# Optimization experiments

Hardware: AMD Instinct MI355X
Metric: run time of the kernel (lower is better)

## Reference

```python
import jax, jax.numpy as jnp
import numpy as np

MARGIN_SCALE = 0.2
SPATIAL_ALPHA = 0.6
CHANNEL_ALPHA = 0.5
LANG_ALPHA = 0.4
EPS = 1e-06


def _xywh_to_xyxy(boxes):
    xc, yc, w, h = jnp.split(boxes, 4, axis=-1)
    return jnp.concatenate([xc - w / 2.0, yc - h / 2.0, xc + w / 2.0, yc + h / 2.0], axis=-1)


def _clamp_boxes(boxes):
    x1, y1, x2, y2 = [jnp.clip(b[..., 0], 0.0, 1.0) for b in jnp.split(boxes, 4, axis=-1)]
    x_low, x_high = jnp.minimum(x1, x2), jnp.maximum(x1, x2)
    y_low, y_high = jnp.minimum(y1, y2), jnp.maximum(y1, y2)
    w = jnp.maximum(x_high - x_low, EPS)
    h = jnp.maximum(y_high - y_low, EPS)
    cx = (x_high + x_low) * 0.5
    cy = (y_high + y_low) * 0.5
    return jnp.stack([
        jnp.clip(cx - w * 0.5, 0.0, 1.0),
        jnp.clip(cy - h * 0.5, 0.0, 1.0),
        jnp.clip(cx + w * 0.5, 0.0, 1.0),
        jnp.clip(cy + h * 0.5, 0.0, 1.0),
    ], axis=-1)


def _box_to_mask(boxes_xyxy, H, W, margin, dtype):
    # fully vectorized replacement of the per-sample Python loop
    ys = jnp.linspace(0.0, 1.0, H)  # [H]
    xs = jnp.linspace(0.0, 1.0, W)  # [W]
    x1, y1, x2, y2 = [boxes_xyxy[:, i] for i in range(4)]
    mx1 = jnp.clip(x1 - margin, 0.0, 1.0)[:, None, None]
    my1 = jnp.clip(y1 - margin, 0.0, 1.0)[:, None, None]
    mx2 = jnp.clip(x2 + margin, 0.0, 1.0)[:, None, None]
    my2 = jnp.clip(y2 + margin, 0.0, 1.0)[:, None, None]
    xg = xs[None, None, :]  # [1,1,W]
    yg = ys[None, :, None]  # [1,H,1]
    mask = (xg >= mx1) & (xg <= mx2) & (yg >= my1) & (yg <= my2)  # [B,H,W]
    return mask.astype(dtype)[:, None, :, :]  # [B,1,H,W]


def _conv2d(x, w, b, pad):
    out = jax.lax.conv_general_dilated(
        x, w, window_strides=(1, 1), padding=((pad, pad), (pad, pad)),
        dimension_numbers=('NCHW', 'OIHW', 'NCHW'))
    return out + b[None, :, None, None]


def setup_inputs() -> dict:
    key = jax.random.key(0)
    ks = jax.random.split(key, 9)
    B, C, H, W = 32, 256, 64, 64
    s = lambda fan_in: 1.0 / np.sqrt(fan_in)
    return {
        'feat': jax.random.normal(ks[0], (B, C, H, W), jnp.float32),
        'lang_vec': jax.random.normal(ks[1], (B, 256), jnp.float32),
        'pointer_xywh': jax.random.uniform(ks[2], (B, 4), jnp.float32),
        'conv1_w': jax.random.normal(ks[3], (16, 1, 3, 3), jnp.float32) * s(9),
        'conv1_b': jnp.zeros((16,), jnp.float32),
        'conv2_w': jax.random.normal(ks[4], (1, 16, 1, 1), jnp.float32) * s(16),
        'conv2_b': jnp.zeros((1,), jnp.float32),
        'cg_w1': jax.random.normal(ks[5], (256, 512), jnp.float32) * s(512),
        'cg_b1': jnp.zeros((256,), jnp.float32),
        'cg_w2': jax.random.normal(ks[6], (256, 256), jnp.float32) * s(256),
        'cg_b2': jnp.zeros((256,), jnp.float32),
        'lf_w1': jax.random.normal(ks[7], (256, 512), jnp.float32) * s(512),
        'lf_b1': jnp.zeros((256,), jnp.float32),
        'lf_w2': jax.random.normal(ks[8], (256, 256), jnp.float32) * s(256),
        'lf_b2': jnp.zeros((256,), jnp.float32),
    }


def reference(feat, lang_vec, pointer_xywh, conv1_w, conv1_b, conv2_w, conv2_b,
              cg_w1, cg_b1, cg_w2, cg_b2, lf_w1, lf_b1, lf_w2, lf_b2):
    B, C, H, W = feat.shape
    boxes_xyxy = _clamp_boxes(_xywh_to_xyxy(pointer_xywh))
    w = jnp.maximum(boxes_xyxy[:, 2] - boxes_xyxy[:, 0], 1e-4)
    h = jnp.maximum(boxes_xyxy[:, 3] - boxes_xyxy[:, 1], 1e-4)
    diag = jnp.sqrt(w * w + h * h)
    margin = jnp.clip(diag * MARGIN_SCALE, 0.02, 0.2)
    mask = _box_to_mask(boxes_xyxy, H, W, margin, feat.dtype)  # [B,1,H,W]

    # spatial gate: conv3x3 -> relu -> conv1x1 -> sigmoid
    hidden = jax.nn.relu(_conv2d(mask, conv1_w, conv1_b, pad=1))
    refined_mask = jax.nn.sigmoid(_conv2d(hidden, conv2_w, conv2_b, pad=0))  # [B,1,H,W]

    mask_area = jnp.maximum(refined_mask.sum(axis=(2, 3)), 1.0)  # [B,1]
    pointer_feat = (feat * refined_mask).sum(axis=(2, 3)) / mask_area  # [B,C]

    fusion = jnp.concatenate([pointer_feat, lang_vec], axis=1)  # [B, C+256]
    ch_gate = jax.nn.sigmoid(jax.nn.relu(fusion @ cg_w1.T + cg_b1) @ cg_w2.T + cg_b2)
    ch_gate = ch_gate.reshape(B, C, 1, 1)
    lang_delta = jnp.tanh(jax.nn.relu(fusion @ lf_w1.T + lf_b1) @ lf_w2.T + lf_b2)

    guided_feat = feat * (1.0 + SPATIAL_ALPHA * refined_mask) * (1.0 + CHANNEL_ALPHA * ch_gate)
    guided_lang = lang_vec + LANG_ALPHA * lang_delta
    return (guided_feat, guided_lang, boxes_xyxy, refined_mask, pointer_feat)
```

## Files before the change

### kernel.cpp

```cpp
#include <hip/hip_runtime.h>
#include <math.h>

#define B_  32
#define C_  256
#define H_  64
#define W_  64
#define HW  (H_*W_)
#define HW4 (HW/4)
#define RPB 4

typedef float f32x4 __attribute__((ext_vector_type(4)));

__device__ __forceinline__ float clamp01(float v) {
    return fminf(fmaxf(v, 0.0f), 1.0f);
}

struct BoxParams {
    float bx1, by1, bx2, by2, mx1, my1, mx2, my2;
};

__device__ __forceinline__ BoxParams box_math(const float* __restrict__ xywh, int b) {
    const float xc = xywh[b * 4 + 0];
    const float yc = xywh[b * 4 + 1];
    const float bw = xywh[b * 4 + 2];
    const float bh = xywh[b * 4 + 3];

    float x1 = clamp01(xc - bw * 0.5f);
    float y1 = clamp01(yc - bh * 0.5f);
    float x2 = clamp01(xc + bw * 0.5f);
    float y2 = clamp01(yc + bh * 0.5f);
    float xl = fminf(x1, x2), xh = fmaxf(x1, x2);
    float yl = fminf(y1, y2), yh = fmaxf(y1, y2);
    float w_ = fmaxf(xh - xl, 1e-6f);
    float h_ = fmaxf(yh - yl, 1e-6f);
    float cx = (xh + xl) * 0.5f, cy = (yh + yl) * 0.5f;
    BoxParams p;
    p.bx1 = clamp01(cx - w_ * 0.5f);
    p.by1 = clamp01(cy - h_ * 0.5f);
    p.bx2 = clamp01(cx + w_ * 0.5f);
    p.by2 = clamp01(cy + h_ * 0.5f);
    float ww = fmaxf(p.bx2 - p.bx1, 1e-4f);
    float hh = fmaxf(p.by2 - p.by1, 1e-4f);
    float diag = sqrtf(ww * ww + hh * hh);
    float margin = fminf(fmaxf(diag * 0.2f, 0.02f), 0.2f);
    p.mx1 = clamp01(p.bx1 - margin);
    p.my1 = clamp01(p.by1 - margin);
    p.mx2 = clamp01(p.bx2 + margin);
    p.my2 = clamp01(p.by2 + margin);
    return p;
}

__device__ __forceinline__ void build_tables(
    int t, const BoxParams& p, float b2v,
    const float* sw1, const float* sb1, const float* sw2,
    int* xpat, int* ypat, float* tbl)
{
    if (t < 64) {
        const int x = t;
        int pp = 0;
        #pragma unroll
        for (int k = 0; k < 3; ++k) {
            const int xx = x + k - 1;
            float gx = (float)((double)xx / 63.0);
            bool in = (xx >= 0) && (xx < W_) && (gx >= p.mx1) && (gx <= p.mx2);
            pp |= (in ? 1 : 0) << k;
        }
        xpat[x] = pp;
    } else if (t < 128) {
        const int y = t - 64;
        int pp = 0;
        #pragma unroll
        for (int k = 0; k < 3; ++k) {
            const int yy = y + k - 1;
            float gy = (float)((double)yy / 63.0);
            bool in = (yy >= 0) && (yy < H_) && (gy >= p.my1) && (gy <= p.my2);
            pp |= (in ? 1 : 0) << k;
        }
        ypat[y] = pp;
    } else if (t < 192) {
        const int e = t - 128;
        const int xp = e & 7, yp = e >> 3;
        float mv[9];
        #pragma unroll
        for (int ky = 0; ky < 3; ++ky)
            #pragma unroll
            for (int kx = 0; kx < 3; ++kx)
                mv[ky * 3 + kx] = (((yp >> ky) & 1) && ((xp >> kx) & 1)) ? 1.0f : 0.0f;
        float z = b2v;
        #pragma unroll
        for (int oc = 0; oc < 16; ++oc) {
            float hsum = sb1[oc];
            #pragma unroll
            for (int k = 0; k < 9; ++k) hsum = fmaf(mv[k], sw1[oc * 9 + k], hsum);
            z = fmaf(fmaxf(hsum, 0.0f), sw2[oc], z);
        }
        tbl[e] = 1.0f / (1.0f + expf(-z));
    }
}

__global__ __launch_bounds__(256) void kern_pf(
    const float* __restrict__ feat, const float* __restrict__ xywh,
    const float* __restrict__ conv1_w, const float* __restrict__ conv1_b,
    const float* __restrict__ conv2_w, const float* __restrict__ conv2_b,
    float* __restrict__ out_boxes, float* __restrict__ out_rm,
    float* __restrict__ out_pf)
{
    const int blk = blockIdx.x;
    const int b = blk >> 6;
    const int g = blk & 63;
    const int c0 = g * RPB;
    const int t = threadIdx.x;

    __shared__ float sw1[16 * 9];
    __shared__ float sb1[16];
    __shared__ float sw2[16];
    __shared__ float tbl[64];
    __shared__ int   xpat[64];
    __shared__ int   ypat[64];
    __shared__ f32x4 rm4_lds[HW4];
    __shared__ float sreda[4];
    __shared__ f32x4 sredv[4];

    float* rm_lds = (float*)rm4_lds;

    if (t < 144)                 sw1[t]       = conv1_w[t];
    else if (t < 160)            sb1[t - 144] = conv1_b[t - 144];
    else if (t < 176)            sw2[t - 160] = conv2_w[t - 160];
    const float b2v = conv2_b[0];

    const BoxParams bp = box_math(xywh, b);
    if (t == 0 && g == 0) {
        out_boxes[b * 4 + 0] = bp.bx1;
        out_boxes[b * 4 + 1] = bp.by1;
        out_boxes[b * 4 + 2] = bp.bx2;
        out_boxes[b * 4 + 3] = bp.by2;
    }
    __syncthreads();

    build_tables(t, bp, b2v, sw1, sb1, sw2, xpat, ypat, tbl);
    __syncthreads();

    float asum = 0.0f;
    for (int p = t; p < HW; p += 256) {
        const int y = p >> 6;
        const int x = p & 63;
        float rm = tbl[ypat[y] * 8 + xpat[x]];
        rm_lds[p] = rm;
        asum += rm;
    }
    #pragma unroll
    for (int off = 32; off > 0; off >>= 1) asum += __shfl_down(asum, off, 64);
    const int lane = t & 63, wid = t >> 6;
    if (lane == 0) sreda[wid] = asum;
    __syncthreads();
    const float inv = 1.0f / fmaxf(sreda[0] + sreda[1] + sreda[2] + sreda[3], 1.0f);

    if (g == 0) {
        f32x4* orm = (f32x4*)(out_rm + (size_t)b * HW);
        for (int i = t; i < HW4; i += 256) orm[i] = rm4_lds[i];
    }

    const f32x4* fr = (const f32x4*)(feat + ((size_t)b * C_ + c0) * HW);
    float s0 = 0.f, s1 = 0.f, s2 = 0.f, s3 = 0.f;
    #pragma unroll 2
    for (int i = t; i < HW4; i += 256) {
        f32x4 r = rm4_lds[i];
        f32x4 f0 = fr[i];
        f32x4 f1 = fr[i + HW4];
        f32x4 f2 = fr[i + 2 * HW4];
        f32x4 f3 = fr[i + 3 * HW4];
        s0 = fmaf(f0.x, r.x, fmaf(f0.y, r.y, fmaf(f0.z, r.z, fmaf(f0.w, r.w, s0))));
        s1 = fmaf(f1.x, r.x, fmaf(f1.y, r.y, fmaf(f1.z, r.z, fmaf(f1.w, r.w, s1))));
        s2 = fmaf(f2.x, r.x, fmaf(f2.y, r.y, fmaf(f2.z, r.z, fmaf(f2.w, r.w, s2))));
        s3 = fmaf(f3.x, r.x, fmaf(f3.y, r.y, fmaf(f3.z, r.z, fmaf(f3.w, r.w, s3))));
    }
    #pragma unroll
    for (int off = 32; off > 0; off >>= 1) {
        s0 += __shfl_down(s0, off, 64);
        s1 += __shfl_down(s1, off, 64);
        s2 += __shfl_down(s2, off, 64);
        s3 += __shfl_down(s3, off, 64);
    }
    if (lane == 0) { f32x4 v; v.x = s0; v.y = s1; v.z = s2; v.w = s3; sredv[wid] = v; }
    __syncthreads();
    if (t == 0) {
        f32x4 t0 = sredv[0], t1 = sredv[1], t2 = sredv[2], t3 = sredv[3];
        out_pf[b * C_ + c0 + 0] = (t0.x + t1.x + t2.x + t3.x) * inv;
        out_pf[b * C_ + c0 + 1] = (t0.y + t1.y + t2.y + t3.y) * inv;
        out_pf[b * C_ + c0 + 2] = (t0.z + t1.z + t2.z + t3.z) * inv;
        out_pf[b * C_ + c0 + 3] = (t0.w + t1.w + t2.w + t3.w) * inv;
    }
}

__global__ __launch_bounds__(256) void kern_mlp(
    const float* __restrict__ pf, const float* __restrict__ lang,
    const float* __restrict__ cg_w1, const float* __restrict__ cg_b1,
    const float* __restrict__ cg_w2, const float* __restrict__ cg_b2,
    const float* __restrict__ lf_w1, const float* __restrict__ lf_b1,
    const float* __restrict__ lf_w2, const float* __restrict__ lf_b2,
    float* __restrict__ ws_cg, float* __restrict__ out_gl)
{
    const int b = blockIdx.x >> 1;
    const int which = blockIdx.x & 1;
    const int t = threadIdx.x;
    __shared__ float fus[512];
    __shared__ float hid[256];

    fus[t]       = pf[b * 256 + t];
    fus[256 + t] = lang[b * 256 + t];

    const float* w1 = which ? lf_w1 : cg_w1;
    const float* b1 = which ? lf_b1 : cg_b1;
    const float* w2 = which ? lf_w2 : cg_w2;
    const float* b2 = which ? lf_b2 : cg_b2;
    __syncthreads();

    const f32x4* wv = (const f32x4*)(w1 + (size_t)t * 512);
    const f32x4* fv = (const f32x4*)fus;
    float s = 0.0f;
    #pragma unroll 4
    for (int k = 0; k < 128; ++k) {
        f32x4 f = fv[k], w = wv[k];
        s = fmaf(f.x, w.x, fmaf(f.y, w.y, fmaf(f.z, w.z, fmaf(f.w, w.w, s))));
    }
    hid[t] = fmaxf(s + b1[t], 0.0f);
    __syncthreads();

    const f32x4* w2v = (const f32x4*)(w2 + (size_t)t * 256);
    const f32x4* hv = (const f32x4*)hid;
    float s2 = 0.0f;
    #pragma unroll 4
    for (int k = 0; k < 64; ++k) {
        f32x4 h = hv[k], w = w2v[k];
        s2 = fmaf(h.x, w.x, fmaf(h.y, w.y, fmaf(h.z, w.z, fmaf(h.w, w.w, s2))));
    }
    s2 += b2[t];
    if (which == 0) {
        ws_cg[b * 256 + t] = 1.0f + 0.5f / (1.0f + expf(-s2));
    } else {
        out_gl[b * 256 + t] = fus[256 + t] + 0.4f * tanhf(s2);
    }
}

__global__ __launch_bounds__(256) void kern_guided(
    const float* __restrict__ feat, const float* __restrict__ rm,
    const float* __restrict__ ws_cg, float* __restrict__ out_gf)
{
    const int blk = blockIdx.x;
    const int b = blk >> 6;
    const int c0 = (blk & 63) * RPB;
    const float g0 = ws_cg[b * C_ + c0 + 0];
    const float g1 = ws_cg[b * C_ + c0 + 1];
    const float g2 = ws_cg[b * C_ + c0 + 2];
    const float g3 = ws_cg[b * C_ + c0 + 3];

    const size_t row0 = ((size_t)b * C_ + c0) * HW;
    const f32x4* fr = (const f32x4*)(feat + row0);
    f32x4* orow = (f32x4*)(out_gf + row0);
    const f32x4* r4 = (const f32x4*)(rm + (size_t)b * HW);

    #pragma unroll 2
    for (int i = threadIdx.x; i < HW4; i += 256) {
        f32x4 r = r4[i];
        f32x4 m;
        m.x = 1.0f + 0.6f * r.x;
        m.y = 1.0f + 0.6f * r.y;
        m.z = 1.0f + 0.6f * r.z;
        m.w = 1.0f + 0.6f * r.w;
        f32x4 f0 = fr[i];
        f32x4 f1 = fr[i + HW4];
        f32x4 f2 = fr[i + 2 * HW4];
        f32x4 f3 = fr[i + 3 * HW4];
        f32x4 o0, o1, o2, o3;
        o0.x = f0.x * m.x * g0; o0.y = f0.y * m.y * g0;
        o0.z = f0.z * m.z * g0; o0.w = f0.w * m.w * g0;
        o1.x = f1.x * m.x * g1; o1.y = f1.y * m.y * g1;
        o1.z = f1.z * m.z * g1; o1.w = f1.w * m.w * g1;
        o2.x = f2.x * m.x * g2; o2.y = f2.y * m.y * g2;
        o2.z = f2.z * m.z * g2; o2.w = f2.w * m.w * g2;
        o3.x = f3.x * m.x * g3; o3.y = f3.y * m.y * g3;
        o3.z = f3.z * m.z * g3; o3.w = f3.w * m.w * g3;
        orow[i]           = o0;
        orow[i + HW4]     = o1;
        orow[i + 2*HW4]   = o2;
        orow[i + 3*HW4]   = o3;
    }
}

extern "C" void kernel_launch(void* const* d_in, const int* in_sizes, int n_in,
                              void* d_out, int out_size, void* d_ws, size_t ws_size,
                              hipStream_t stream) {
    const float* feat     = (const float*)d_in[0];
    const float* lang     = (const float*)d_in[1];
    const float* xywh     = (const float*)d_in[2];
    const float* conv1_w  = (const float*)d_in[3];
    const float* conv1_b  = (const float*)d_in[4];
    const float* conv2_w  = (const float*)d_in[5];
    const float* conv2_b  = (const float*)d_in[6];
    const float* cg_w1    = (const float*)d_in[7];
    const float* cg_b1    = (const float*)d_in[8];
    const float* cg_w2    = (const float*)d_in[9];
    const float* cg_b2    = (const float*)d_in[10];
    const float* lf_w1    = (const float*)d_in[11];
    const float* lf_b1    = (const float*)d_in[12];
    const float* lf_w2    = (const float*)d_in[13];
    const float* lf_b2    = (const float*)d_in[14];

    float* out = (float*)d_out;
    const size_t N_GF = (size_t)B_ * C_ * HW;
    float* out_gf    = out;
    float* out_gl    = out_gf + N_GF;
    float* out_boxes = out_gl + (size_t)B_ * C_;
    float* out_rm    = out_boxes + B_ * 4;
    float* out_pf    = out_rm + (size_t)B_ * HW;

    float* wsf   = (float*)d_ws;
    float* ws_cg = wsf;

    (void)ws_size; (void)in_sizes; (void)n_in; (void)out_size;

    kern_pf<<<B_ * C_ / RPB, 256, 0, stream>>>(feat, xywh,
                                               conv1_w, conv1_b, conv2_w, conv2_b,
                                               out_boxes, out_rm, out_pf);
    kern_mlp<<<B_ * 2, 256, 0, stream>>>(out_pf, lang,
                                         cg_w1, cg_b1, cg_w2, cg_b2,
                                         lf_w1, lf_b1, lf_w2, lf_b2,
                                         ws_cg, out_gl);
    kern_guided<<<B_ * C_ / RPB, 256, 0, stream>>>(feat, out_rm, ws_cg, out_gf);
}
```

Measured before the change: 96.61 us.

## Split mask into separate kernel, swizzle block order, use nontemporal stores

Moves refined-mask construction and area reduction into a small kernel that writes the mask and per-quarter partial sums to global memory, so the pointer-feature kernel reads the mask from memory instead of rebuilding it in LDS in every block. Both feat-streaming kernels remap block indices so that consecutive blocks land on different batches, and the loops are fully unrolled with more loads in flight. The guided-output kernel writes with nontemporal stores so the large output does not pollute cache. The cost is one extra kernel launch and a global round trip for the mask, and the swizzle may hurt cache reuse of the shared mask row.

```diff
diff --git a/kernel.cpp b/kernel.cpp
--- a/kernel.cpp
+++ b/kernel.cpp
@@ -13,6 +13,10 @@
 
 __device__ __forceinline__ float clamp01(float v) {
     return fminf(fmaxf(v, 0.0f), 1.0f);
+}
+
+__device__ __forceinline__ int swz2048(int blk) {
+    return (blk & 7) * 256 + (blk >> 3);
 }
 
 struct BoxParams {
@@ -98,17 +102,15 @@
     }
 }
 
-__global__ __launch_bounds__(256) void kern_pf(
-    const float* __restrict__ feat, const float* __restrict__ xywh,
+__global__ __launch_bounds__(256) void kern_mask(
+    const float* __restrict__ xywh,
     const float* __restrict__ conv1_w, const float* __restrict__ conv1_b,
     const float* __restrict__ conv2_w, const float* __restrict__ conv2_b,
     float* __restrict__ out_boxes, float* __restrict__ out_rm,
-    float* __restrict__ out_pf)
-{
-    const int blk = blockIdx.x;
-    const int b = blk >> 6;
-    const int g = blk & 63;
-    const int c0 = g * RPB;
+    float* __restrict__ ws_part)
+{
+    const int b = blockIdx.x >> 2;
+    const int q = blockIdx.x & 3;
     const int t = threadIdx.x;
 
     __shared__ float sw1[16 * 9];
@@ -117,11 +119,7 @@
     __shared__ float tbl[64];
     __shared__ int   xpat[64];
     __shared__ int   ypat[64];
-    __shared__ f32x4 rm4_lds[HW4];
-    __shared__ float sreda[4];
-    __shared__ f32x4 sredv[4];
-
-    float* rm_lds = (float*)rm4_lds;
+    __shared__ float sred[4];
 
     if (t < 144)                 sw1[t]       = conv1_w[t];
     else if (t < 160)            sb1[t - 144] = conv1_b[t - 144];
@@ -129,7 +127,7 @@
     const float b2v = conv2_b[0];
 
     const BoxParams bp = box_math(xywh, b);
-    if (t == 0 && g == 0) {
+    if (t == 0 && q == 0) {
         out_boxes[b * 4 + 0] = bp.bx1;
         out_boxes[b * 4 + 1] = bp.by1;
         out_boxes[b * 4 + 2] = bp.bx2;
@@ -141,39 +139,61 @@
     __syncthreads();
 
     float asum = 0.0f;
-    for (int p = t; p < HW; p += 256) {
+    const int p0 = q * 1024;
+    for (int pi = t; pi < 1024; pi += 256) {
+        const int p = p0 + pi;
         const int y = p >> 6;
         const int x = p & 63;
         float rm = tbl[ypat[y] * 8 + xpat[x]];
-        rm_lds[p] = rm;
+        out_rm[b * HW + p] = rm;
         asum += rm;
     }
     #pragma unroll
     for (int off = 32; off > 0; off >>= 1) asum += __shfl_down(asum, off, 64);
-    const int lane = t & 63, wid = t >> 6;
-    if (lane == 0) sreda[wid] = asum;
-    __syncthreads();
-    const float inv = 1.0f / fmaxf(sreda[0] + sreda[1] + sreda[2] + sreda[3], 1.0f);
-
-    if (g == 0) {
-        f32x4* orm = (f32x4*)(out_rm + (size_t)b * HW);
-        for (int i = t; i < HW4; i += 256) orm[i] = rm4_lds[i];
-    }
+    int lane = t & 63, wid = t >> 6;
+    if (lane == 0) sred[wid] = asum;
+    __syncthreads();
+    if (t == 0) ws_part[b * 4 + q] = sred[0] + sred[1] + sred[2] + sred[3];
+}
+
+__global__ __launch_bounds__(256) void kern_pf(
+    const float* __restrict__ feat, const float* __restrict__ rm,
+    const float* __restrict__ ws_part, float* __restrict__ out_pf)
+{
+    const int job = swz2048(blockIdx.x);
+    const int b = job >> 6;
+    const int c0 = (job & 63) * RPB;
+    const int t = threadIdx.x;
+    __shared__ f32x4 sredv[4];
 
     const f32x4* fr = (const f32x4*)(feat + ((size_t)b * C_ + c0) * HW);
+    const f32x4* r4 = (const f32x4*)(rm + (size_t)b * HW);
+
     float s0 = 0.f, s1 = 0.f, s2 = 0.f, s3 = 0.f;
-    #pragma unroll 2
-    for (int i = t; i < HW4; i += 256) {
-        f32x4 r = rm4_lds[i];
-        f32x4 f0 = fr[i];
-        f32x4 f1 = fr[i + HW4];
-        f32x4 f2 = fr[i + 2 * HW4];
-        f32x4 f3 = fr[i + 3 * HW4];
-        s0 = fmaf(f0.x, r.x, fmaf(f0.y, r.y, fmaf(f0.z, r.z, fmaf(f0.w, r.w, s0))));
-        s1 = fmaf(f1.x, r.x, fmaf(f1.y, r.y, fmaf(f1.z, r.z, fmaf(f1.w, r.w, s1))));
-        s2 = fmaf(f2.x, r.x, fmaf(f2.y, r.y, fmaf(f2.z, r.z, fmaf(f2.w, r.w, s2))));
-        s3 = fmaf(f3.x, r.x, fmaf(f3.y, r.y, fmaf(f3.z, r.z, fmaf(f3.w, r.w, s3))));
-    }
+    #pragma unroll
+    for (int k = 0; k < 2; ++k) {
+        const int i0 = t + k * 512;
+        const int i1 = i0 + 256;
+        f32x4 ra = r4[i0];
+        f32x4 rb = r4[i1];
+        f32x4 a0 = fr[i0];
+        f32x4 a1 = fr[i0 + HW4];
+        f32x4 a2 = fr[i0 + 2 * HW4];
+        f32x4 a3 = fr[i0 + 3 * HW4];
+        f32x4 b0 = fr[i1];
+        f32x4 b1 = fr[i1 + HW4];
+        f32x4 b2 = fr[i1 + 2 * HW4];
+        f32x4 b3 = fr[i1 + 3 * HW4];
+        s0 = fmaf(a0.x, ra.x, fmaf(a0.y, ra.y, fmaf(a0.z, ra.z, fmaf(a0.w, ra.w, s0))));
+        s1 = fmaf(a1.x, ra.x, fmaf(a1.y, ra.y, fmaf(a1.z, ra.z, fmaf(a1.w, ra.w, s1))));
+        s2 = fmaf(a2.x, ra.x, fmaf(a2.y, ra.y, fmaf(a2.z, ra.z, fmaf(a2.w, ra.w, s2))));
+        s3 = fmaf(a3.x, ra.x, fmaf(a3.y, ra.y, fmaf(a3.z, ra.z, fmaf(a3.w, ra.w, s3))));
+        s0 = fmaf(b0.x, rb.x, fmaf(b0.y, rb.y, fmaf(b0.z, rb.z, fmaf(b0.w, rb.w, s0))));
+        s1 = fmaf(b1.x, rb.x, fmaf(b1.y, rb.y, fmaf(b1.z, rb.z, fmaf(b1.w, rb.w, s1))));
+        s2 = fmaf(b2.x, rb.x, fmaf(b2.y, rb.y, fmaf(b2.z, rb.z, fmaf(b2.w, rb.w, s2))));
+        s3 = fmaf(b3.x, rb.x, fmaf(b3.y, rb.y, fmaf(b3.z, rb.z, fmaf(b3.w, rb.w, s3))));
+    }
+
     #pragma unroll
     for (int off = 32; off > 0; off >>= 1) {
         s0 += __shfl_down(s0, off, 64);
@@ -181,9 +201,13 @@
         s2 += __shfl_down(s2, off, 64);
         s3 += __shfl_down(s3, off, 64);
     }
+    const int lane = t & 63, wid = t >> 6;
     if (lane == 0) { f32x4 v; v.x = s0; v.y = s1; v.z = s2; v.w = s3; sredv[wid] = v; }
     __syncthreads();
     if (t == 0) {
+        float area = fmaxf(ws_part[b * 4 + 0] + ws_part[b * 4 + 1] +
+                           ws_part[b * 4 + 2] + ws_part[b * 4 + 3], 1.0f);
+        float inv = 1.0f / area;
         f32x4 t0 = sredv[0], t1 = sredv[1], t2 = sredv[2], t3 = sredv[3];
         out_pf[b * C_ + c0 + 0] = (t0.x + t1.x + t2.x + t3.x) * inv;
         out_pf[b * C_ + c0 + 1] = (t0.y + t1.y + t2.y + t3.y) * inv;
@@ -246,9 +270,10 @@
     const float* __restrict__ feat, const float* __restrict__ rm,
     const float* __restrict__ ws_cg, float* __restrict__ out_gf)
 {
-    const int blk = blockIdx.x;
-    const int b = blk >> 6;
-    const int c0 = (blk & 63) * RPB;
+    const int job = swz2048(blockIdx.x);
+    const int b = job >> 6;
+    const int c0 = (job & 63) * RPB;
+    const int t = threadIdx.x;
     const float g0 = ws_cg[b * C_ + c0 + 0];
     const float g1 = ws_cg[b * C_ + c0 + 1];
     const float g2 = ws_cg[b * C_ + c0 + 2];
@@ -259,31 +284,52 @@
     f32x4* orow = (f32x4*)(out_gf + row0);
     const f32x4* r4 = (const f32x4*)(rm + (size_t)b * HW);
 
-    #pragma unroll 2
-    for (int i = threadIdx.x; i < HW4; i += 256) {
-        f32x4 r = r4[i];
-        f32x4 m;
-        m.x = 1.0f + 0.6f * r.x;
-        m.y = 1.0f + 0.6f * r.y;
-        m.z = 1.0f + 0.6f * r.z;
-        m.w = 1.0f + 0.6f * r.w;
-        f32x4 f0 = fr[i];
-        f32x4 f1 = fr[i + HW4];
-        f32x4 f2 = fr[i + 2 * HW4];
-        f32x4 f3 = fr[i + 3 * HW4];
-        f32x4 o0, o1, o2, o3;
-        o0.x = f0.x * m.x * g0; o0.y = f0.y * m.y * g0;
-        o0.z = f0.z * m.z * g0; o0.w = f0.w * m.w * g0;
-        o1.x = f1.x * m.x * g1; o1.y = f1.y * m.y * g1;
-        o1.z = f1.z * m.z * g1; o1.w = f1.w * m.w * g1;
-        o2.x = f2.x * m.x * g2; o2.y = f2.y * m.y * g2;
-        o2.z = f2.z * m.z * g2; o2.w = f2.w * m.w * g2;
-        o3.x = f3.x * m.x * g3; o3.y = f3.y * m.y * g3;
-        o3.z = f3.z * m.z * g3; o3.w = f3.w * m.w * g3;
-        orow[i]           = o0;
-        orow[i + HW4]     = o1;
-        orow[i + 2*HW4]   = o2;
-        orow[i + 3*HW4]   = o3;
+    #pragma unroll
+    for (int k = 0; k < 2; ++k) {
+        const int i0 = t + k * 512;
+        const int i1 = i0 + 256;
+        f32x4 ra = r4[i0];
+        f32x4 rb = r4[i1];
+        f32x4 a0 = fr[i0];
+        f32x4 a1 = fr[i0 + HW4];
+        f32x4 a2 = fr[i0 + 2 * HW4];
+        f32x4 a3 = fr[i0 + 3 * HW4];
+        f32x4 b0 = fr[i1];
+        f32x4 b1 = fr[i1 + HW4];
+        f32x4 b2 = fr[i1 + 2 * HW4];
+        f32x4 b3 = fr[i1 + 3 * HW4];
+
+        f32x4 ma, mb;
+        ma.x = 1.0f + 0.6f * ra.x; ma.y = 1.0f + 0.6f * ra.y;
+        ma.z = 1.0f + 0.6f * ra.z; ma.w = 1.0f + 0.6f * ra.w;
+        mb.x = 1.0f + 0.6f * rb.x; mb.y = 1.0f + 0.6f * rb.y;
+        mb.z = 1.0f + 0.6f * rb.z; mb.w = 1.0f + 0.6f * rb.w;
+
+        f32x4 o;
+        o.x = a0.x * ma.x * g0; o.y = a0.y * ma.y * g0;
+        o.z = a0.z * ma.z * g0; o.w = a0.w * ma.w * g0;
+        __builtin_nontemporal_store(o, &orow[i0]);
+        o.x = a1.x * ma.x * g1; o.y = a1.y * ma.y * g1;
+        o.z = a1.z * ma.z * g1; o.w = a1.w * ma.w * g1;
+        __builtin_nontemporal_store(o, &orow[i0 + HW4]);
+        o.x = a2.x * ma.x * g2; o.y = a2.y * ma.y * g2;
+        o.z = a2.z * ma.z * g2; o.w = a2.w * ma.w * g2;
+        __builtin_nontemporal_store(o, &orow[i0 + 2 * HW4]);
+        o.x = a3.x * ma.x * g3; o.y = a3.y * ma.y * g3;
+        o.z = a3.z * ma.z * g3; o.w = a3.w * ma.w * g3;
+        __builtin_nontemporal_store(o, &orow[i0 + 3 * HW4]);
+        o.x = b0.x * mb.x * g0; o.y = b0.y * mb.y * g0;
+        o.z = b0.z * mb.z * g0; o.w = b0.w * mb.w * g0;
+        __builtin_nontemporal_store(o, &orow[i1]);
+        o.x = b1.x * mb.x * g1; o.y = b1.y * mb.y * g1;
+        o.z = b1.z * mb.z * g1; o.w = b1.w * mb.w * g1;
+        __builtin_nontemporal_store(o, &orow[i1 + HW4]);
+        o.x = b2.x * mb.x * g2; o.y = b2.y * mb.y * g2;
+        o.z = b2.z * mb.z * g2; o.w = b2.w * mb.w * g2;
+        __builtin_nontemporal_store(o, &orow[i1 + 2 * HW4]);
+        o.x = b3.x * mb.x * g3; o.y = b3.y * mb.y * g3;
+        o.z = b3.z * mb.z * g3; o.w = b3.w * mb.w * g3;
+        __builtin_nontemporal_store(o, &orow[i1 + 3 * HW4]);
     }
 }
 
@@ -314,14 +360,15 @@
     float* out_rm    = out_boxes + B_ * 4;
     float* out_pf    = out_rm + (size_t)B_ * HW;
 
-    float* wsf   = (float*)d_ws;
-    float* ws_cg = wsf;
+    float* wsf     = (float*)d_ws;
+    float* ws_part = wsf;
+    float* ws_cg   = wsf + 128;
 
     (void)ws_size; (void)in_sizes; (void)n_in; (void)out_size;
 
-    kern_pf<<<B_ * C_ / RPB, 256, 0, stream>>>(feat, xywh,
-                                               conv1_w, conv1_b, conv2_w, conv2_b,
-                                               out_boxes, out_rm, out_pf);
+    kern_mask<<<B_ * 4, 256, 0, stream>>>(xywh, conv1_w, conv1_b, conv2_w, conv2_b,
+                                          out_boxes, out_rm, ws_part);
+    kern_pf<<<B_ * C_ / RPB, 256, 0, stream>>>(feat, out_rm, ws_part, out_pf);
     kern_mlp<<<B_ * 2, 256, 0, stream>>>(out_pf, lang,
                                          cg_w1, cg_b1, cg_w2, cg_b2,
                                          lf_w1, lf_b1, lf_w2, lf_b2,
```

Measured after the change: 102.0 us. +5.6%, slower.

## Recompute refined mask in guided kernel and use nontemporal stores

Applied to the files above, without the earlier changes.

The guided kernel now rebuilds the refined mask in LDS from the box parameters and conv weights instead of reading it back from global memory, precomputing 1+0.6*rm. Both the pointer-feature and guided loops are fully unrolled so each thread issues all 16 feature loads up front, and the output writes use nontemporal stores to limit cache pollution. This costs extra per-block setup (table build plus LDS fill and syncs) and more registers in exchange for more loads in flight and less global traffic.

```diff
diff --git a/kernel.cpp b/kernel.cpp
--- a/kernel.cpp
+++ b/kernel.cpp
@@ -98,6 +98,20 @@
     }
 }
 
+__device__ __forceinline__ float fill_rm(
+    int t, const int* xpat, const int* ypat, const float* tbl, float* rm_lds)
+{
+    float asum = 0.0f;
+    for (int p = t; p < HW; p += 256) {
+        const int y = p >> 6;
+        const int x = p & 63;
+        float rm = tbl[ypat[y] * 8 + xpat[x]];
+        rm_lds[p] = rm;
+        asum += rm;
+    }
+    return asum;
+}
+
 __global__ __launch_bounds__(256) void kern_pf(
     const float* __restrict__ feat, const float* __restrict__ xywh,
     const float* __restrict__ conv1_w, const float* __restrict__ conv1_b,
@@ -140,14 +154,7 @@
     build_tables(t, bp, b2v, sw1, sb1, sw2, xpat, ypat, tbl);
     __syncthreads();
 
-    float asum = 0.0f;
-    for (int p = t; p < HW; p += 256) {
-        const int y = p >> 6;
-        const int x = p & 63;
-        float rm = tbl[ypat[y] * 8 + xpat[x]];
-        rm_lds[p] = rm;
-        asum += rm;
-    }
+    float asum = fill_rm(t, xpat, ypat, tbl, rm_lds);
     #pragma unroll
     for (int off = 32; off > 0; off >>= 1) asum += __shfl_down(asum, off, 64);
     const int lane = t & 63, wid = t >> 6;
@@ -160,20 +167,27 @@
         for (int i = t; i < HW4; i += 256) orm[i] = rm4_lds[i];
     }
 
-    const f32x4* fr = (const f32x4*)(feat + ((size_t)b * C_ + c0) * HW);
+    const f32x4* fs = (const f32x4*)(feat + ((size_t)b * C_ + c0) * HW);
     float s0 = 0.f, s1 = 0.f, s2 = 0.f, s3 = 0.f;
-    #pragma unroll 2
-    for (int i = t; i < HW4; i += 256) {
-        f32x4 r = rm4_lds[i];
-        f32x4 f0 = fr[i];
-        f32x4 f1 = fr[i + HW4];
-        f32x4 f2 = fr[i + 2 * HW4];
-        f32x4 f3 = fr[i + 3 * HW4];
-        s0 = fmaf(f0.x, r.x, fmaf(f0.y, r.y, fmaf(f0.z, r.z, fmaf(f0.w, r.w, s0))));
-        s1 = fmaf(f1.x, r.x, fmaf(f1.y, r.y, fmaf(f1.z, r.z, fmaf(f1.w, r.w, s1))));
-        s2 = fmaf(f2.x, r.x, fmaf(f2.y, r.y, fmaf(f2.z, r.z, fmaf(f2.w, r.w, s2))));
-        s3 = fmaf(f3.x, r.x, fmaf(f3.y, r.y, fmaf(f3.z, r.z, fmaf(f3.w, r.w, s3))));
-    }
+    #pragma unroll
+    for (int r = 0; r < 4; ++r) {
+        f32x4 f0 = fs[t + (r * 4 + 0) * 256];
+        f32x4 f1 = fs[t + (r * 4 + 1) * 256];
+        f32x4 f2 = fs[t + (r * 4 + 2) * 256];
+        f32x4 f3 = fs[t + (r * 4 + 3) * 256];
+        f32x4 r0 = rm4_lds[t];
+        f32x4 r1 = rm4_lds[t + 256];
+        f32x4 r2 = rm4_lds[t + 512];
+        f32x4 r3 = rm4_lds[t + 768];
+        float acc = 0.0f;
+        acc = fmaf(f0.x, r0.x, fmaf(f0.y, r0.y, fmaf(f0.z, r0.z, fmaf(f0.w, r0.w, acc))));
+        acc = fmaf(f1.x, r1.x, fmaf(f1.y, r1.y, fmaf(f1.z, r1.z, fmaf(f1.w, r1.w, acc))));
+        acc = fmaf(f2.x, r2.x, fmaf(f2.y, r2.y, fmaf(f2.z, r2.z, fmaf(f2.w, r2.w, acc))));
+        acc = fmaf(f3.x, r3.x, fmaf(f3.y, r3.y, fmaf(f3.z, r3.z, fmaf(f3.w, r3.w, acc))));
+        if (r == 0) s0 = acc; else if (r == 1) s1 = acc;
+        else if (r == 2) s2 = acc; else s3 = acc;
+    }
+
     #pragma unroll
     for (int off = 32; off > 0; off >>= 1) {
         s0 += __shfl_down(s0, off, 64);
@@ -243,47 +257,75 @@
 }
 
 __global__ __launch_bounds__(256) void kern_guided(
-    const float* __restrict__ feat, const float* __restrict__ rm,
+    const float* __restrict__ feat, const float* __restrict__ xywh,
+    const float* __restrict__ conv1_w, const float* __restrict__ conv1_b,
+    const float* __restrict__ conv2_w, const float* __restrict__ conv2_b,
     const float* __restrict__ ws_cg, float* __restrict__ out_gf)
 {
     const int blk = blockIdx.x;
     const int b = blk >> 6;
     const int c0 = (blk & 63) * RPB;
+    const int t = threadIdx.x;
+
+    __shared__ float sw1[16 * 9];
+    __shared__ float sb1[16];
+    __shared__ float sw2[16];
+    __shared__ float tbl[64];
+    __shared__ int   xpat[64];
+    __shared__ int   ypat[64];
+    __shared__ f32x4 rm4_lds[HW4];
+
+    float* rm_lds = (float*)rm4_lds;
+
+    if (t < 144)                 sw1[t]       = conv1_w[t];
+    else if (t < 160)            sb1[t - 144] = conv1_b[t - 144];
+    else if (t < 176)            sw2[t - 160] = conv2_w[t - 160];
+    const float b2v = conv2_b[0];
+
+    const BoxParams bp = box_math(xywh, b);
+    __syncthreads();
+    build_tables(t, bp, b2v, sw1, sb1, sw2, xpat, ypat, tbl);
+    __syncthreads();
+    for (int p = t; p < HW; p += 256) {
+        const int y = p >> 6;
+        const int x = p & 63;
+        rm_lds[p] = 1.0f + 0.6f * tbl[ypat[y] * 8 + xpat[x]];
+    }
+    __syncthreads();
+
     const float g0 = ws_cg[b * C_ + c0 + 0];
     const float g1 = ws_cg[b * C_ + c0 + 1];
     const float g2 = ws_cg[b * C_ + c0 + 2];
     const float g3 = ws_cg[b * C_ + c0 + 3];
 
     const size_t row0 = ((size_t)b * C_ + c0) * HW;
-    const f32x4* fr = (const f32x4*)(feat + row0);
-    f32x4* orow = (f32x4*)(out_gf + row0);
-    const f32x4* r4 = (const f32x4*)(rm + (size_t)b * HW);
-
-    #pragma unroll 2
-    for (int i = threadIdx.x; i < HW4; i += 256) {
-        f32x4 r = r4[i];
-        f32x4 m;
-        m.x = 1.0f + 0.6f * r.x;
-        m.y = 1.0f + 0.6f * r.y;
-        m.z = 1.0f + 0.6f * r.z;
-        m.w = 1.0f + 0.6f * r.w;
-        f32x4 f0 = fr[i];
-        f32x4 f1 = fr[i + HW4];
-        f32x4 f2 = fr[i + 2 * HW4];
-        f32x4 f3 = fr[i + 3 * HW4];
-        f32x4 o0, o1, o2, o3;
-        o0.x = f0.x * m.x * g0; o0.y = f0.y * m.y * g0;
-        o0.z = f0.z * m.z * g0; o0.w = f0.w * m.w * g0;
-        o1.x = f1.x * m.x * g1; o1.y = f1.y * m.y * g1;
-        o1.z = f1.z * m.z * g1; o1.w = f1.w * m.w * g1;
-        o2.x = f2.x * m.x * g2; o2.y = f2.y * m.y * g2;
-        o2.z = f2.z * m.z * g2; o2.w = f2.w * m.w * g2;
-        o3.x = f3.x * m.x * g3; o3.y = f3.y * m.y * g3;
-        o3.z = f3.z * m.z * g3; o3.w = f3.w * m.w * g3;
-        orow[i]           = o0;
-        orow[i + HW4]     = o1;
-        orow[i + 2*HW4]   = o2;
-        orow[i + 3*HW4]   = o3;
+    const f32x4* fs = (const f32x4*)(feat + row0);
+    f32x4* os = (f32x4*)(out_gf + row0);
+
+    #pragma unroll
+    for (int r = 0; r < 4; ++r) {
+        const float gr = (r == 0) ? g0 : (r == 1) ? g1 : (r == 2) ? g2 : g3;
+        f32x4 f0 = fs[t + (r * 4 + 0) * 256];
+        f32x4 f1 = fs[t + (r * 4 + 1) * 256];
+        f32x4 f2 = fs[t + (r * 4 + 2) * 256];
+        f32x4 f3 = fs[t + (r * 4 + 3) * 256];
+        f32x4 m0 = rm4_lds[t];
+        f32x4 m1 = rm4_lds[t + 256];
+        f32x4 m2 = rm4_lds[t + 512];
+        f32x4 m3 = rm4_lds[t + 768];
+        f32x4 o;
+        o.x = f0.x * m0.x * gr; o.y = f0.y * m0.y * gr;
+        o.z = f0.z * m0.z * gr; o.w = f0.w * m0.w * gr;
+        __builtin_nontemporal_store(o, &os[t + (r * 4 + 0) * 256]);
+        o.x = f1.x * m1.x * gr; o.y = f1.y * m1.y * gr;
+        o.z = f1.z * m1.z * gr; o.w = f1.w * m1.w * gr;
+        __builtin_nontemporal_store(o, &os[t + (r * 4 + 1) * 256]);
+        o.x = f2.x * m2.x * gr; o.y = f2.y * m2.y * gr;
+        o.z = f2.z * m2.z * gr; o.w = f2.w * m2.w * gr;
+        __builtin_nontemporal_store(o, &os[t + (r * 4 + 2) * 256]);
+        o.x = f3.x * m3.x * gr; o.y = f3.y * m3.y * gr;
+        o.z = f3.z * m3.z * gr; o.w = f3.w * m3.w * gr;
+        __builtin_nontemporal_store(o, &os[t + (r * 4 + 3) * 256]);
     }
 }
 
@@ -326,5 +368,7 @@
                                          cg_w1, cg_b1, cg_w2, cg_b2,
                                          lf_w1, lf_b1, lf_w2, lf_b2,
                                          ws_cg, out_gl);
-    kern_guided<<<B_ * C_ / RPB, 256, 0, stream>>>(feat, out_rm, ws_cg, out_gf);
-}
+    kern_guided<<<B_ * C_ / RPB, 256, 0, stream>>>(feat, xywh,
+                                                   conv1_w, conv1_b, conv2_w, conv2_b,
+                                                   ws_cg, out_gf);
+}
```

Measured after the change: 97.03 us. No clear change (+0.4%).
